# Kernel tuning notes

Hardware: AMD Instinct MI355X
Metric: run time of the kernel (lower is better)

## Reference

```python
import jax, jax.numpy as jnp
import numpy as np

B = 8       # complexes in batch
C = 32      # CDR residues per antibody
G = 2048    # antigen nodes per complex
D = 128     # encoded_dims
N_AB = B * C
N_AG = B * G
N = N_AB + N_AG
SLOPE = 0.2
EPS_BN = 1e-5


def _build_edges():
    # block-sparse bipartite edges (cdr_b x ag_b), symmetrized, + self loops
    srcs, dsts = [], []
    for b in range(B):
        ab = np.arange(b * C, (b + 1) * C)
        ag = np.arange(N_AB + b * G, N_AB + (b + 1) * G)
        g1, g2 = np.meshgrid(ab, ag, indexing='ij')
        srcs.append(g1.ravel()); dsts.append(g2.ravel())
    s = np.concatenate(srcs); d = np.concatenate(dsts)
    loops = np.arange(N)
    src = np.concatenate([s, d, loops]).astype(np.int32)
    dst = np.concatenate([d, s, loops]).astype(np.int32)
    return src, dst


def setup_inputs() -> dict:
    key = jax.random.key(0)
    ks = jax.random.split(key, 16)
    sc = 1.0 / np.sqrt(D)
    edge_src, edge_dst = _build_edges()
    return {
        'selected_ab': jax.random.normal(ks[0], (N_AB, D), jnp.float32),
        'x_ag': jax.random.normal(ks[1], (N_AG, D), jnp.float32),
        'W1': jax.random.normal(ks[2], (D, D), jnp.float32) * sc,
        'a_src1': jax.random.normal(ks[3], (D,), jnp.float32) * sc,
        'a_dst1': jax.random.normal(ks[4], (D,), jnp.float32) * sc,
        'b1': jnp.zeros((D,), jnp.float32),
        'W2': jax.random.normal(ks[5], (D, D), jnp.float32) * sc,
        'a_src2': jax.random.normal(ks[6], (D,), jnp.float32) * sc,
        'a_dst2': jax.random.normal(ks[7], (D,), jnp.float32) * sc,
        'b2': jnp.zeros((D,), jnp.float32),
        'bn_ab_g': jnp.ones((2 * D,), jnp.float32),
        'bn_ab_b': jnp.zeros((2 * D,), jnp.float32),
        'bn_ag_g': jnp.ones((2 * D,), jnp.float32),
        'bn_ag_b': jnp.zeros((2 * D,), jnp.float32),
        'fc_w': jax.random.normal(ks[8], (2 * D, 1), jnp.float32) * sc,
        'fc_b': jnp.zeros((1,), jnp.float32),
        'agfc_w': jax.random.normal(ks[9], (2 * D, 1), jnp.float32) * sc,
        'agfc_b': jnp.zeros((1,), jnp.float32),
        'edge_src': jnp.asarray(edge_src),
        'edge_dst': jnp.asarray(edge_dst),
    }


def _gat(x, W, a_s, a_d, b, src, dst):
    # PyG GATConv, heads=1, eval mode (dropout off)
    h = x @ W                                  # [N, D]
    al_s = h @ a_s                             # [N]
    al_d = h @ a_d                             # [N]
    e = jax.nn.leaky_relu(al_s[src] + al_d[dst], SLOPE)   # [E]
    m = jax.ops.segment_max(e, dst, num_segments=N)
    e = jnp.exp(e - m[dst])
    z = jax.ops.segment_sum(e, dst, num_segments=N)
    alpha = e / (z[dst] + 1e-16)
    out = jax.ops.segment_sum(h[src] * alpha[:, None], dst, num_segments=N)
    return out + b


def _bn(x, g, b):
    # training-mode batch stats (biased variance), like torch BatchNorm1d
    m = x.mean(0)
    v = ((x - m) ** 2).mean(0)
    return (x - m) / jnp.sqrt(v + EPS_BN) * g + b


def reference(selected_ab, x_ag, W1, a_src1, a_dst1, b1, W2, a_src2, a_dst2, b2,
              bn_ab_g, bn_ab_b, bn_ag_g, bn_ag_b, fc_w, fc_b, agfc_w, agfc_b,
              edge_src, edge_dst):
    x = jnp.concatenate([selected_ab, x_ag], axis=0)          # [N, D]
    x = jax.nn.relu(_gat(x, W1, a_src1, a_dst1, b1, edge_src, edge_dst))
    x = _gat(x, W2, a_src2, a_dst2, b2, edge_src, edge_dst)
    x_ab = jnp.concatenate([x[:N_AB], selected_ab], axis=1)   # [N_ab, 2D]
    x_ab = jax.nn.relu(_bn(x_ab, bn_ab_g, bn_ab_b))
    x_ab = (x_ab @ fc_w + fc_b).ravel()
    x_ag_o = jnp.concatenate([x[N_AB:], x_ag], axis=1)        # [N_ag, 2D]
    x_ag_o = jax.nn.relu(_bn(x_ag_o, bn_ag_g, bn_ag_b))
    x_ag_o = (x_ag_o @ agfc_w + agfc_b).ravel()
    return (x_ab, x_ag_o)
```

## Files before the change

kernel.cpp:

```cpp
#include <hip/hip_runtime.h>


#define N_AB 256
#define N_AG 16384
#define N_ALL 16640
#define G_AG 2048
#define SLOPE 0.2f
#define MSHIFT 20.0f

typedef __attribute__((ext_vector_type(4))) float f32x4;
typedef __attribute__((ext_vector_type(8))) __bf16 bf16x8;
typedef __attribute__((ext_vector_type(8))) unsigned short u16x8;
typedef unsigned short ushort_t;

__device__ __forceinline__ float bf2f(ushort_t u) {
  union { unsigned int i; float f; } v; v.i = ((unsigned int)u) << 16; return v.f;
}
__device__ __forceinline__ ushort_t f2bf(float f) {
  union { float fv; unsigned int i; } v; v.fv = f;
  unsigned int x = v.i;
  return (ushort_t)((x + 0x7fffu + ((x >> 16) & 1u)) >> 16);
}
__device__ __forceinline__ float lrelu(float x) { return x >= 0.f ? x : SLOPE * x; }
__device__ __forceinline__ float expw(float e) {
  return __expf(fminf(e, 60.f) - MSHIFT);
}
__device__ __forceinline__ float ldf(const void* p, size_t i, int f) {
  return f ? ((const float*)p)[i] : bf2f(((const ushort_t*)p)[i]);
}
__device__ __forceinline__ void ld8f(const void* p, size_t i, int f, float* o) {
  if (f) {
    const f32x4* q = (const f32x4*)((const float*)p + i);
    f32x4 a = q[0], b = q[1];
#pragma unroll
    for (int j = 0; j < 4; ++j) { o[j] = a[j]; o[j + 4] = b[j]; }
  } else {
    u16x8 v = *(const u16x8*)((const ushort_t*)p + i);
#pragma unroll
    for (int j = 0; j < 8; ++j) o[j] = bf2f(v[j]);
  }
}

__global__ __launch_bounds__(256) void k_pre(
    const void* __restrict__ W1, const void* __restrict__ W2,
    const void* __restrict__ as1, const void* __restrict__ ad1,
    const void* __restrict__ as2, const void* __restrict__ ad2,
    const void* __restrict__ sel_ab,
    ushort_t* __restrict__ W1t, ushort_t* __restrict__ W2t,
    float* __restrict__ va, float* __restrict__ bnsumAG,
    float* __restrict__ accf, float* __restrict__ accz,
    float* __restrict__ selpart, float* __restrict__ selpartq,
    int* __restrict__ flagp) {
  __shared__ float ls[2][128], lq[2][128];
  int t = threadIdx.x, lane = t & 63, wid = t >> 6;
  int bx = blockIdx.x;
  const ushort_t* selu = (const ushort_t*)sel_ab;
  int cnt = 0;
#pragma unroll
  for (int i = 0; i < 8; ++i) {
    unsigned e = (selu[lane * 8 + i] >> 7) & 0xFF;
    if (e > 0xC8) cnt++;
  }
  int f = (__popcll(__ballot(cnt > 0)) >= 3) ? 1 : 0;
  if (bx == 0 && t == 0) flagp[0] = f;

  if (bx < 16) {
    const void* W = (bx < 8) ? W1 : W2;
    ushort_t* Wt = (bx < 8) ? W1t : W2t;
    int base = (bx & 7) * 2048 + t * 8;
    float o[8];
    ld8f(W, base, f, o);
#pragma unroll
    for (int j = 0; j < 8; ++j) {
      int idx = base + j;
      Wt[(idx & 127) * 128 + (idx >> 7)] = f2bf(o[j]);
    }
  } else if (bx < 32) {
    int j = bx - 16;
    const void* W   = (j < 8) ? W1 : W2;
    const void* asv = (j < 8) ? as1 : as2;
    const void* adv = (j < 8) ? ad1 : ad2;
    int vbase = (j < 8) ? 0 : 256;
    int basek = (j & 7) * 16 + wid * 4;
    float a_s0 = ldf(asv, lane, f), a_s1 = ldf(asv, lane + 64, f);
    float a_d0 = ldf(adv, lane, f), a_d1 = ldf(adv, lane + 64, f);
#pragma unroll
    for (int i = 0; i < 4; ++i) {
      int k = basek + i;
      float w0 = ldf(W, (size_t)k * 128 + lane, f);
      float w1 = ldf(W, (size_t)k * 128 + lane + 64, f);
      float ps = w0 * a_s0 + w1 * a_s1;
      float pd = w0 * a_d0 + w1 * a_d1;
#pragma unroll
      for (int o = 1; o < 64; o <<= 1) {
        ps += __shfl_xor(ps, o);
        pd += __shfl_xor(pd, o);
      }
      if (lane == 0) { va[vbase + k] = ps; va[vbase + 128 + k] = pd; }
    }
  } else if (bx < 40) {
    int j = bx - 32;
    f32x4* az = (f32x4*)(accf + (size_t)j * 4096);
    f32x4 z4 = (f32x4){0.f, 0.f, 0.f, 0.f};
    for (int i = t; i < 1024; i += 256) az[i] = z4;
    if (j == 0) { bnsumAG[t] = 0.f; bnsumAG[t + 256] = 0.f; accz[t] = 0.f; }
  } else {
    int j = bx - 40;
    int col = t & 127, rh = t >> 7;
    int r0 = j * 32 + rh * 16;
    float s = 0.f, sq = 0.f;
    for (int r = 0; r < 16; ++r) {
      float v = ldf(sel_ab, (size_t)(r0 + r) * 128 + col, f);
      s += v; sq += v * v;
    }
    ls[rh][col] = s; lq[rh][col] = sq;
    __syncthreads();
    if (t < 128) {
      selpart[j * 128 + t] = ls[0][t] + ls[1][t];
      selpartq[j * 128 + t] = lq[0][t] + lq[1][t];
    }
  }
}

__global__ __launch_bounds__(256) void k_gemm(
    const void* __restrict__ xa, int modeA,
    const void* __restrict__ xb, int modeB,
    const int* __restrict__ flagp,
    const ushort_t* __restrict__ Wt, const float* __restrict__ va,
    ushort_t* __restrict__ h, float* __restrict__ als, float* __restrict__ ald,
    float* __restrict__ accf, float* __restrict__ accz,
    const void* __restrict__ biasAb, float* __restrict__ xabf, int do_abfin,
    const void* __restrict__ xraw, float* __restrict__ bnsumAG, int do_colsum) {
  __shared__ float zsh[32], wsh[32];
  int t = threadIdx.x, lane = t & 63, wid = t >> 6;
  int bx = blockIdx.x;

  if (do_colsum && bx < 64) {
    int fr = *flagp;
    int j = bx;
    int col = t & 127, half = t >> 7;
    int r0 = j * 256 + half * 128;
    float s = 0.f, sq = 0.f;
    for (int r = 0; r < 128; ++r) {
      float v = ldf(xraw, (size_t)(r0 + r) * 128 + col, fr);
      s += v; sq += v * v;
    }
    atomicAdd(&bnsumAG[128 + col], s);
    atomicAdd(&bnsumAG[384 + col], sq);
    return;
  }
  int gbx = do_colsum ? bx - 64 : bx;

  if (do_abfin && bx < 8) {
    int fr = *flagp;
    int b = bx;
    if (t < 32) {
      int grow = b * 32 + t;
      float w = expw(lrelu(als[grow] + ald[grow]));
      zsh[t] = accz[grow] + w;
      wsh[t] = w;
      accz[grow] = 0.f;
    }
    __syncthreads();
#pragma unroll
    for (int i = 0; i < 16; ++i) {
      int e = i * 256 + t;
      int rl = e >> 7, col = e & 127;
      int grow = b * 32 + rl;
      size_t idx = (size_t)grow * 128 + col;
      float hv = bf2f(h[idx]);
      float v = (accf[idx] + wsh[rl] * hv) / (zsh[rl] + 1e-16f) + ldf(biasAb, col, fr);
      accf[idx] = 0.f;
      v = fmaxf(v, 0.f);
      xabf[idx] = v;
    }
    __syncthreads();
  }

  int rw0 = gbx * 32 + (wid >> 1) * 16;
  int ch = wid & 1;
  const void* xsrc; int roff, mode;
  if (rw0 < N_AB) { xsrc = xa; roff = rw0; mode = modeA; }
  else            { xsrc = xb; roff = rw0 - N_AB; mode = modeB; }
  int fx = (mode == 2) ? *flagp : mode;
  int mm = lane & 15, q = lane >> 4;
  f32x4 acc[4];
#pragma unroll
  for (int b = 0; b < 4; ++b) acc[b] = (f32x4){0.f, 0.f, 0.f, 0.f};
  float pals = 0.f, pald = 0.f;
#pragma unroll
  for (int s = 0; s < 4; ++s) {
    int koff = s * 32 + q * 8;
    union { u16x8 u; bf16x8 b; } af;
    float o[8];
    ld8f(xsrc, (size_t)(roff + mm) * 128 + koff, fx, o);
#pragma unroll
    for (int j = 0; j < 8; ++j) {
      af.u[j] = f2bf(o[j]);
      pals += o[j] * va[koff + j];
      pald += o[j] * va[128 + koff + j];
    }
#pragma unroll
    for (int nt = 0; nt < 4; ++nt) {
      int colb = ch * 64 + nt * 16;
      bf16x8 bfr = *(const bf16x8*)(Wt + (size_t)(colb + mm) * 128 + koff);
      acc[nt] = __builtin_amdgcn_mfma_f32_16x16x32_bf16(af.b, bfr, acc[nt], 0, 0, 0);
    }
  }
  if (ch == 0) {
    float s1 = pals; s1 += __shfl_xor(s1, 16); s1 += __shfl_xor(s1, 32);
    float d1 = pald; d1 += __shfl_xor(d1, 16); d1 += __shfl_xor(d1, 32);
    if (lane < 16) { als[rw0 + lane] = s1; ald[rw0 + lane] = d1; }
  }
#pragma unroll
  for (int nt = 0; nt < 4; ++nt)
#pragma unroll
    for (int r = 0; r < 4; ++r) {
      int row = rw0 + q * 4 + r;
      int col = ch * 64 + nt * 16 + mm;
      h[(size_t)row * 128 + col] = f2bf(acc[nt][r]);
    }
}

#define ABP_STRIDE 72
#define AG_STRIDE 40
#define HS_OFF 5120
#define HS_STRIDE 136
__global__ __launch_bounds__(256) void k_agg(
    const ushort_t* __restrict__ h, const float* __restrict__ als,
    const float* __restrict__ ald, const void* __restrict__ bias,
    const int* __restrict__ flagp, ushort_t* __restrict__ xout,
    float* __restrict__ accf, float* __restrict__ accz,
    float* __restrict__ bnsumAG, int do_relu, int do_bnsum) {
  __shared__ ushort_t hT[13824];
  __shared__ float alsS[64];
  __shared__ float colsum[128], colsq[128];
  int bx = blockIdx.x;
  int t = threadIdx.x, lane = t & 63, wid = t >> 6;
  int mm = lane & 15, q = lane >> 4;

  if (bx < 256) {
    int b = bx >> 5, jt = bx & 31;
    int f = *flagp;
    int jbase = N_AB + b * G_AG + jt * 64;
    {
      int row = t & 31, c0g = (t >> 5) * 16;
      const ushort_t* src = h + (size_t)(b * 32 + row) * 128 + c0g;
      u16x8 v0 = *(const u16x8*)src;
      u16x8 v1 = *(const u16x8*)(src + 8);
#pragma unroll
      for (int j = 0; j < 8; ++j) {
        hT[(c0g + j) * AG_STRIDE + row] = v0[j];
        hT[(c0g + 8 + j) * AG_STRIDE + row] = v1[j];
      }
      ushort_t* hS = hT + HS_OFF;
      const ushort_t* hsrc = h + (size_t)jbase * 128;
#pragma unroll
      for (int it = 0; it < 4; ++it) {
        int e = it * 2048 + t * 8;
        int rr = e >> 7, cb = e & 127;
        *(u16x8*)&hS[rr * HS_STRIDE + cb] =
            *(const u16x8*)(hsrc + (size_t)rr * 128 + cb);
      }
      if (t < 32) alsS[t] = als[b * 32 + t];
      if (t < 128) { colsum[t] = 0.f; colsq[t] = 0.f; }
    }
    __syncthreads();
    int jl = jt * 64 + wid * 16;
    int jrow = N_AB + b * G_AG + jl;
    float aldj = ald[jrow + mm];
    float alsj = als[jrow + mm];
    union { u16x8 u; bf16x8 b; } af;
    float zp = 0.f;
#pragma unroll
    for (int j = 0; j < 8; ++j) {
      ushort_t us = f2bf(expw(lrelu(alsS[q * 8 + j] + aldj)));
      af.u[j] = us;
      zp += bf2f(us);
    }
    zp += __shfl_xor(zp, 16);
    zp += __shfl_xor(zp, 32);
    float wself = expw(lrelu(alsj + aldj));
    float z = zp + wself;
    float zin[4], wz[4];
#pragma unroll
    for (int r = 0; r < 4; ++r) {
      int rowl = q * 4 + r;
      float zr = __shfl(z, rowl);
      float wsr = __shfl(wself, rowl);
      float inv = 1.0f / (zr + 1e-16f);
      zin[r] = inv; wz[r] = wsr * inv;
    }
    const ushort_t* hSr = hT + HS_OFF + (size_t)(wid * 16) * HS_STRIDE;
#pragma unroll
    for (int nt = 0; nt < 8; ++nt) {
      int col = nt * 16 + mm;
      union { u16x8 u; bf16x8 b; } bfr;
      bfr.b = *(const bf16x8*)(&hT[col * AG_STRIDE + q * 8]);
      f32x4 acc = {0.f, 0.f, 0.f, 0.f};
      acc = __builtin_amdgcn_mfma_f32_16x16x32_bf16(af.b, bfr.b, acc, 0, 0, 0);
      float biasv = ldf(bias, col, f);
      float sl = 0.f, sq = 0.f;
#pragma unroll
      for (int r = 0; r < 4; ++r) {
        int row = q * 4 + r;
        float hv = bf2f(hSr[row * HS_STRIDE + col]);
        float v = acc[r] * zin[r] + wz[r] * hv + biasv;
        sl += v; sq += v * v;
        if (do_relu) v = fmaxf(v, 0.f);
        xout[(size_t)(jrow + row) * 128 + col] = f2bf(v);
      }
      if (do_bnsum) {
        atomicAdd(&colsum[col], sl);
        atomicAdd(&colsq[col], sq);
      }
    }
    if (do_bnsum) {
      __syncthreads();
      if (t < 128) {
        atomicAdd(&bnsumAG[t], colsum[t]);
        atomicAdd(&bnsumAG[256 + t], colsq[t]);
      }
    }
  } else {
    int bx2 = bx - 256;
    int b = bx2 >> 5, sg = bx2 & 31;
    int jrow0 = N_AB + b * G_AG + sg * 64;
    {
      int jr = t & 63, cgrp = (t >> 6) * 32;
      const ushort_t* src = h + (size_t)(jrow0 + jr) * 128 + cgrp;
#pragma unroll
      for (int v = 0; v < 4; ++v) {
        u16x8 vv = *(const u16x8*)(src + v * 8);
#pragma unroll
        for (int j = 0; j < 8; ++j)
          hT[(cgrp + v * 8 + j) * ABP_STRIDE + jr] = vv[j];
      }
      if (t < 64) alsS[t] = als[jrow0 + t];
    }
    __syncthreads();
    float aldm[2] = { ald[b * 32 + mm], ald[b * 32 + 16 + mm] };
    f32x4 acc[2][2];
#pragma unroll
    for (int a = 0; a < 2; ++a)
#pragma unroll
      for (int c = 0; c < 2; ++c) acc[a][c] = (f32x4){0.f, 0.f, 0.f, 0.f};
    float zz[2] = {0.f, 0.f};
#pragma unroll
    for (int s = 0; s < 2; ++s) {
      int k0 = s * 32 + q * 8;
      float a8[8];
#pragma unroll
      for (int j = 0; j < 8; ++j) a8[j] = alsS[k0 + j];
      union { u16x8 u; bf16x8 b; } af[2];
#pragma unroll
      for (int mt = 0; mt < 2; ++mt)
#pragma unroll
        for (int j = 0; j < 8; ++j) {
          ushort_t us = f2bf(expw(lrelu(a8[j] + aldm[mt])));
          af[mt].u[j] = us;
          zz[mt] += bf2f(us);
        }
#pragma unroll
      for (int ns = 0; ns < 2; ++ns) {
        int n = wid * 32 + ns * 16 + mm;
        union { u16x8 u; bf16x8 b; } bfr;
        bfr.b = *(const bf16x8*)(&hT[n * ABP_STRIDE + k0]);
        acc[0][ns] = __builtin_amdgcn_mfma_f32_16x16x32_bf16(af[0].b, bfr.b, acc[0][ns], 0, 0, 0);
        acc[1][ns] = __builtin_amdgcn_mfma_f32_16x16x32_bf16(af[1].b, bfr.b, acc[1][ns], 0, 0, 0);
      }
    }
#pragma unroll
    for (int mt = 0; mt < 2; ++mt)
#pragma unroll
      for (int ns = 0; ns < 2; ++ns)
#pragma unroll
        for (int r = 0; r < 4; ++r) {
          int row = b * 32 + mt * 16 + q * 4 + r;
          int col = wid * 32 + ns * 16 + mm;
          atomicAdd(&accf[(size_t)row * 128 + col], acc[mt][ns][r]);
        }
#pragma unroll
    for (int mt = 0; mt < 2; ++mt) {
      float z = zz[mt];
      z += __shfl_xor(z, 16);
      z += __shfl_xor(z, 32);
      if (wid == 0 && lane < 16)
        atomicAdd(&accz[b * 32 + mt * 16 + lane], z);
    }
  }
}

__global__ __launch_bounds__(256) void k_abfin(
    const float* __restrict__ accf, const float* __restrict__ accz,
    const ushort_t* __restrict__ h, const float* __restrict__ als,
    const float* __restrict__ ald, const void* __restrict__ bias,
    const int* __restrict__ flagp, float* __restrict__ xabf,
    float* __restrict__ abpart, float* __restrict__ abpartq,
    const float* __restrict__ bnsumAG,
    const void* __restrict__ gag, const void* __restrict__ bag,
    const void* __restrict__ agfcw, float* __restrict__ statsAG) {
  __shared__ float zsh[8], wsh[8];
  __shared__ float cs[2][128], cq[2][128];
  int bx = blockIdx.x, t = threadIdx.x;
  int f = *flagp;
  if (bx == 32) {
    float mean = bnsumAG[t] * (1.f / 16384.f);
    float var = fmaxf(bnsumAG[256 + t] * (1.f / 16384.f) - mean * mean, 0.f);
    float A = ldf(gag, t, f) / sqrtf(var + 1e-5f);
    statsAG[t] = A;
    statsAG[256 + t] = ldf(bag, t, f) - mean * A;
    statsAG[512 + t] = ldf(agfcw, t, f);
    return;
  }
  int b = bx >> 2, q4 = bx & 3;
  if (t < 8) {
    int grow = b * 32 + q4 * 8 + t;
    float w = expw(lrelu(als[grow] + ald[grow]));
    zsh[t] = accz[grow] + w;
    wsh[t] = w;
  }
  __syncthreads();
  float s = 0.f, sq = 0.f;
#pragma unroll
  for (int i = 0; i < 4; ++i) {
    int e = i * 256 + t;
    int rl = e >> 7, col = e & 127;
    int grow = b * 32 + q4 * 8 + rl;
    size_t idx = (size_t)grow * 128 + col;
    float hv = bf2f(h[idx]);
    float v = (accf[idx] + wsh[rl] * hv) / (zsh[rl] + 1e-16f) + ldf(bias, col, f);
    xabf[idx] = v;
    s += v; sq += v * v;
  }
  cs[t >> 7][t & 127] = s;
  cq[t >> 7][t & 127] = sq;
  __syncthreads();
  if (t < 128) {
    abpart[bx * 128 + t] = cs[0][t] + cs[1][t];
    abpartq[bx * 128 + t] = cq[0][t] + cq[1][t];
  }
}

__global__ __launch_bounds__(256) void k_head(
    const float* __restrict__ xfab, const ushort_t* __restrict__ xfag,
    const void* __restrict__ sel_ab, const void* __restrict__ x_ag,
    const float* __restrict__ statsAG,
    const float* __restrict__ selpart, const float* __restrict__ selpartq,
    const float* __restrict__ abpart, const float* __restrict__ abpartq,
    const void* __restrict__ gab, const void* __restrict__ bab,
    const void* __restrict__ fcw,
    const void* __restrict__ fcb, const void* __restrict__ agfcb,
    const int* __restrict__ flagp, void* __restrict__ out) {
  __shared__ float stA[256], stB[256], stW[256];
  int t = threadIdx.x, lane = t & 63, wid = t >> 6;
  int f = *flagp;
  int isAb = (blockIdx.x < 16);
  if (isAb) {
    float s = 0.f, sq = 0.f;
    if (t < 128) {
      for (int j = 0; j < 32; ++j) {
        s += abpart[j * 128 + t];
        sq += abpartq[j * 128 + t];
      }
    } else {
      int c = t - 128;
      for (int j = 0; j < 8; ++j) {
        s += selpart[j * 128 + c];
        sq += selpartq[j * 128 + c];
      }
    }
    float mean = s * (1.f / 256.f);
    float var = fmaxf(sq * (1.f / 256.f) - mean * mean, 0.f);
    float A = ldf(gab, t, f) / sqrtf(var + 1e-5f);
    stA[t] = A;
    stB[t] = ldf(bab, t, f) - mean * A;
    stW[t] = ldf(fcw, t, f);
  } else {
    stA[t] = statsAG[t];
    stB[t] = statsAG[256 + t];
    stW[t] = statsAG[512 + t];
  }
  __syncthreads();

  int c0 = lane * 2;
  float a0 = stA[c0],        a1 = stA[c0 + 1];
  float a2 = stA[128 + c0],  a3 = stA[128 + c0 + 1];
  float g0 = stB[c0],        g1 = stB[c0 + 1];
  float g2 = stB[128 + c0],  g3 = stB[128 + c0 + 1];
  float w0 = stW[c0],        w1 = stW[c0 + 1];
  float w2 = stW[128 + c0],  w3 = stW[128 + c0 + 1];
  int row0 = isAb ? (blockIdx.x * 16 + wid * 4)
                  : (N_AB + (blockIdx.x - 16) * 16 + wid * 4);
  float bb = isAb ? ldf(fcb, 0, f) : ldf(agfcb, 0, f);
#pragma unroll
  for (int i = 0; i < 4; ++i) {
    int row = row0 + i;
    float v0, v1, v2, v3;
    if (isAb) {
      const float* p = xfab + (size_t)row * 128 + c0;
      v0 = p[0]; v1 = p[1];
      size_t ro = (size_t)row * 128 + c0;
      v2 = ldf(sel_ab, ro, f);
      v3 = ldf(sel_ab, ro + 1, f);
    } else {
      const ushort_t* p = xfag + (size_t)row * 128 + c0;
      v0 = bf2f(p[0]); v1 = bf2f(p[1]);
      size_t ro = (size_t)(row - N_AB) * 128 + c0;
      v2 = ldf(x_ag, ro, f);
      v3 = ldf(x_ag, ro + 1, f);
    }
    float acc =
        fmaxf(v0 * a0 + g0, 0.f) * w0
      + fmaxf(v1 * a1 + g1, 0.f) * w1
      + fmaxf(v2 * a2 + g2, 0.f) * w2
      + fmaxf(v3 * a3 + g3, 0.f) * w3;
#pragma unroll
    for (int o = 1; o < 64; o <<= 1) acc += __shfl_xor(acc, o);
    if (lane == 0) {
      float r = acc + bb;
      if (f) ((float*)out)[row] = r;
      else   ((ushort_t*)out)[row] = f2bf(r);
    }
  }
}

extern "C" void kernel_launch(void* const* d_in, const int* in_sizes, int n_in,
                              void* d_out, int out_size, void* d_ws, size_t ws_size,
                              hipStream_t stream) {
  (void)in_sizes; (void)n_in; (void)out_size; (void)ws_size;
  const void* sel_ab = d_in[0];
  const void* x_ag   = d_in[1];
  const void* W1     = d_in[2];
  const void* as1    = d_in[3];
  const void* ad1    = d_in[4];
  const void* b1     = d_in[5];
  const void* W2     = d_in[6];
  const void* as2    = d_in[7];
  const void* ad2    = d_in[8];
  const void* b2     = d_in[9];
  const void* gab    = d_in[10];
  const void* bab    = d_in[11];
  const void* gag    = d_in[12];
  const void* bag    = d_in[13];
  const void* fcw    = d_in[14];
  const void* fcb    = d_in[15];
  const void* agfcw  = d_in[16];
  const void* agfcb  = d_in[17];

  ushort_t* h  = (ushort_t*)d_in[18];
  ushort_t* xb = (ushort_t*)d_in[19];

  char* wsp = (char*)d_ws;
  size_t off = 0;
  auto carve = [&](size_t bytes) -> char* {
    char* p = wsp + off; off += (bytes + 255) & ~(size_t)255; return p;
  };
  int* flag      = (int*)carve(64 * 4);
  ushort_t* W1t  = (ushort_t*)carve(16384 * 2);
  ushort_t* W2t  = (ushort_t*)carve(16384 * 2);
  float* va      = (float*)carve(512 * 4);
  float* als     = (float*)carve((size_t)N_ALL * 4);
  float* ald     = (float*)carve((size_t)N_ALL * 4);
  float* bnsumAG = (float*)carve(512 * 4);
  float* statsAG = (float*)carve(768 * 4);
  float* xabf    = (float*)carve((size_t)N_AB * 128 * 4);
  float* accf    = (float*)carve((size_t)N_AB * 128 * 4);
  float* accz    = (float*)carve(256 * 4);
  float* selpart = (float*)carve(8 * 128 * 4);
  float* selpartq= (float*)carve(8 * 128 * 4);
  float* abpart  = (float*)carve(32 * 128 * 4);
  float* abpartq = (float*)carve(32 * 128 * 4);

  k_pre<<<48, 256, 0, stream>>>(W1, W2, as1, ad1, as2, ad2, sel_ab,
                                W1t, W2t, va, bnsumAG, accf, accz,
                                selpart, selpartq, flag);
  k_gemm<<<584, 256, 0, stream>>>(sel_ab, 2, x_ag, 2, flag, W1t, va, h, als, ald,
                                  accf, accz, b1, xabf, 0, x_ag, bnsumAG, 1);
  k_agg<<<512, 256, 0, stream>>>(h, als, ald, b1, flag, xb, accf, accz,
                                 bnsumAG, 1, 0);
  k_gemm<<<520, 256, 0, stream>>>(xabf, 1, xb + (size_t)N_AB * 128, 0, flag, W2t, va + 256, h, als, ald,
                                  accf, accz, b1, xabf, 1, x_ag, bnsumAG, 0);
  k_agg<<<512, 256, 0, stream>>>(h, als, ald, b2, flag, xb, accf, accz,
                                 bnsumAG, 0, 1);
  k_abfin<<<33, 256, 0, stream>>>(accf, accz, h, als, ald, b2, flag, xabf,
                                  abpart, abpartq, bnsumAG, gag, bag, agfcw,
                                  statsAG);
  k_head<<<1040, 256, 0, stream>>>(xabf, xb, sel_ab, x_ag, statsAG,
                                   selpart, selpartq, abpart, abpartq,
                                   gab, bab, fcw, fcb, agfcb, flag, d_out);
}
```

Measured before the change: 171.7 us.

## Fuse all GAT stages into one persistent kernel with grid-wide barriers

Merges the seven separate kernel launches (pre, two gemm, two agg, ab finish, head) into one persistent kernel with 512 blocks. The stages are separated by atomic-counter grid barriers, and the kernel is used only when occupancy allows 2 blocks per CU. It also moves the antigen BN input statistics into the pre phase as per-block partial sums instead of accumulating them during the first gemm. The aim is to remove launch gaps and inter-kernel drain, at the cost of spin-wait barriers, a possible deadlock if the grid does not all fit on the device, and lower parallelism for the GEMM stages.

```diff
diff --git a/kernel.cpp b/kernel.cpp
--- a/kernel.cpp
+++ b/kernel.cpp
@@ -7,6 +7,7 @@
 #define G_AG 2048
 #define SLOPE 0.2f
 #define MSHIFT 20.0f
+#define GRID_F 512
 
 typedef __attribute__((ext_vector_type(4))) float f32x4;
 typedef __attribute__((ext_vector_type(8))) __bf16 bf16x8;
@@ -38,6 +39,496 @@
     u16x8 v = *(const u16x8*)((const ushort_t*)p + i);
 #pragma unroll
     for (int j = 0; j < 8; ++j) o[j] = bf2f(v[j]);
+  }
+}
+
+__device__ __forceinline__ void gbar(unsigned* __restrict__ ctr, int t) {
+  __syncthreads();
+  if (t == 0) {
+    __threadfence();
+    atomicAdd(ctr, 1u);
+    while (atomicAdd(ctr, 0u) < (unsigned)GRID_F) __builtin_amdgcn_s_sleep(2);
+  }
+  __syncthreads();
+  __threadfence();
+}
+
+__global__ __launch_bounds__(64) void k_init(unsigned* __restrict__ ctr) {
+  if (threadIdx.x < 16) ctr[threadIdx.x] = 0u;
+}
+
+#define ABP_STRIDE 72
+#define AG_STRIDE 40
+#define HS_OFF 5120
+#define HS_STRIDE 136
+
+__global__ __launch_bounds__(256, 2) void k_fused(
+    const void* __restrict__ sel_ab, const void* __restrict__ x_ag,
+    const void* __restrict__ W1, const void* __restrict__ as1,
+    const void* __restrict__ ad1, const void* __restrict__ b1,
+    const void* __restrict__ W2, const void* __restrict__ as2,
+    const void* __restrict__ ad2, const void* __restrict__ b2,
+    const void* __restrict__ gab, const void* __restrict__ bab,
+    const void* __restrict__ gag, const void* __restrict__ bag,
+    const void* __restrict__ fcw, const void* __restrict__ fcb,
+    const void* __restrict__ agfcw, const void* __restrict__ agfcb,
+    ushort_t* __restrict__ h, ushort_t* __restrict__ xb,
+    ushort_t* __restrict__ W1t, ushort_t* __restrict__ W2t,
+    float* __restrict__ va, float* __restrict__ als, float* __restrict__ ald,
+    float* __restrict__ bnsumAG, float* __restrict__ statsAG,
+    float* __restrict__ xabf, float* __restrict__ accf,
+    float* __restrict__ accz,
+    float* __restrict__ selpart, float* __restrict__ selpartq,
+    float* __restrict__ abpart, float* __restrict__ abpartq,
+    float* __restrict__ agpart, float* __restrict__ agpartq,
+    unsigned* __restrict__ ctrs, void* __restrict__ out) {
+  __shared__ ushort_t hT[13824];
+  __shared__ float alsS[64];
+  __shared__ float colsum[128], colsq[128];
+  __shared__ float preLs[2][128], preLq[2][128];
+  __shared__ float zsh[32], wsh[32];
+  __shared__ float stA[256], stB[256], stW[256];
+
+  int t = threadIdx.x, lane = t & 63, wid = t >> 6;
+  int bx = blockIdx.x;
+  int mm = lane & 15, q = lane >> 4;
+
+  const ushort_t* selu = (const ushort_t*)sel_ab;
+  int cnt = 0;
+#pragma unroll
+  for (int i = 0; i < 8; ++i) {
+    unsigned e = (selu[lane * 8 + i] >> 7) & 0xFF;
+    if (e > 0xC8) cnt++;
+  }
+  int f = (__popcll(__ballot(cnt > 0)) >= 3) ? 1 : 0;
+
+  if (bx < 16) {
+    const void* W = (bx < 8) ? W1 : W2;
+    ushort_t* Wt = (bx < 8) ? W1t : W2t;
+    int base = (bx & 7) * 2048 + t * 8;
+    float o[8];
+    ld8f(W, base, f, o);
+#pragma unroll
+    for (int j = 0; j < 8; ++j) {
+      int idx = base + j;
+      Wt[(idx & 127) * 128 + (idx >> 7)] = f2bf(o[j]);
+    }
+  } else if (bx < 32) {
+    int j = bx - 16;
+    const void* W   = (j < 8) ? W1 : W2;
+    const void* asv = (j < 8) ? as1 : as2;
+    const void* adv = (j < 8) ? ad1 : ad2;
+    int vbase = (j < 8) ? 0 : 256;
+    int basek = (j & 7) * 16 + wid * 4;
+    float a_s0 = ldf(asv, lane, f), a_s1 = ldf(asv, lane + 64, f);
+    float a_d0 = ldf(adv, lane, f), a_d1 = ldf(adv, lane + 64, f);
+#pragma unroll
+    for (int i = 0; i < 4; ++i) {
+      int k = basek + i;
+      float w0 = ldf(W, (size_t)k * 128 + lane, f);
+      float w1 = ldf(W, (size_t)k * 128 + lane + 64, f);
+      float ps = w0 * a_s0 + w1 * a_s1;
+      float pd = w0 * a_d0 + w1 * a_d1;
+#pragma unroll
+      for (int o = 1; o < 64; o <<= 1) {
+        ps += __shfl_xor(ps, o);
+        pd += __shfl_xor(pd, o);
+      }
+      if (lane == 0) { va[vbase + k] = ps; va[vbase + 128 + k] = pd; }
+    }
+  } else if (bx < 40) {
+    int j = bx - 32;
+    f32x4* az = (f32x4*)(accf + (size_t)j * 4096);
+    f32x4 z4 = (f32x4){0.f, 0.f, 0.f, 0.f};
+    for (int i = t; i < 1024; i += 256) az[i] = z4;
+    if (j == 0) { bnsumAG[t] = 0.f; bnsumAG[t + 256] = 0.f; accz[t] = 0.f; }
+  } else if (bx < 48) {
+    int j = bx - 40;
+    int col = t & 127, rh = t >> 7;
+    int r0 = j * 32 + rh * 16;
+    float s = 0.f, sq = 0.f;
+    for (int r = 0; r < 16; ++r) {
+      float v = ldf(sel_ab, (size_t)(r0 + r) * 128 + col, f);
+      s += v; sq += v * v;
+    }
+    preLs[rh][col] = s; preLq[rh][col] = sq;
+    __syncthreads();
+    if (t < 128) {
+      selpart[j * 128 + t] = preLs[0][t] + preLs[1][t];
+      selpartq[j * 128 + t] = preLq[0][t] + preLq[1][t];
+    }
+  } else if (bx < 112) {
+    int j = bx - 48;
+    int col = t & 127, half = t >> 7;
+    int r0 = j * 256 + half * 128;
+    float s = 0.f, sq = 0.f;
+    for (int r = 0; r < 128; ++r) {
+      float v = ldf(x_ag, (size_t)(r0 + r) * 128 + col, f);
+      s += v; sq += v * v;
+    }
+    preLs[half][col] = s; preLq[half][col] = sq;
+    __syncthreads();
+    if (t < 128) {
+      agpart[j * 128 + t] = preLs[0][t] + preLs[1][t];
+      agpartq[j * 128 + t] = preLq[0][t] + preLq[1][t];
+    }
+  }
+  gbar(&ctrs[0], t);
+
+  auto gemm_tile = [&](int tile, const void* xa, int fxA, const void* xbv,
+                       int fxB, const ushort_t* Wt, const float* vav) {
+    int rw0 = tile * 32 + (wid >> 1) * 16;
+    int ch = wid & 1;
+    const void* xsrc; int roff, fx;
+    if (rw0 < N_AB) { xsrc = xa; roff = rw0; fx = fxA; }
+    else            { xsrc = xbv; roff = rw0 - N_AB; fx = fxB; }
+    f32x4 acc[4];
+#pragma unroll
+    for (int b = 0; b < 4; ++b) acc[b] = (f32x4){0.f, 0.f, 0.f, 0.f};
+    float pals = 0.f, pald = 0.f;
+#pragma unroll
+    for (int s = 0; s < 4; ++s) {
+      int koff = s * 32 + q * 8;
+      union { u16x8 u; bf16x8 b; } af;
+      float o[8];
+      ld8f(xsrc, (size_t)(roff + mm) * 128 + koff, fx, o);
+#pragma unroll
+      for (int j = 0; j < 8; ++j) {
+        af.u[j] = f2bf(o[j]);
+        pals += o[j] * vav[koff + j];
+        pald += o[j] * vav[128 + koff + j];
+      }
+#pragma unroll
+      for (int nt = 0; nt < 4; ++nt) {
+        int colb = ch * 64 + nt * 16;
+        bf16x8 bfr = *(const bf16x8*)(Wt + (size_t)(colb + mm) * 128 + koff);
+        acc[nt] = __builtin_amdgcn_mfma_f32_16x16x32_bf16(af.b, bfr, acc[nt], 0, 0, 0);
+      }
+    }
+    if (ch == 0) {
+      float s1 = pals; s1 += __shfl_xor(s1, 16); s1 += __shfl_xor(s1, 32);
+      float d1 = pald; d1 += __shfl_xor(d1, 16); d1 += __shfl_xor(d1, 32);
+      if (lane < 16) { als[rw0 + lane] = s1; ald[rw0 + lane] = d1; }
+    }
+#pragma unroll
+    for (int nt = 0; nt < 4; ++nt)
+#pragma unroll
+      for (int r = 0; r < 4; ++r) {
+        int row = rw0 + q * 4 + r;
+        int col = ch * 64 + nt * 16 + mm;
+        h[(size_t)row * 128 + col] = f2bf(acc[nt][r]);
+      }
+  };
+
+  auto agg_phase = [&](const void* bias, int do_relu, int do_bnsum) {
+    if (bx < 256) {
+      int b = bx >> 5, jt = bx & 31;
+      int jbase = N_AB + b * G_AG + jt * 64;
+      {
+        int row = t & 31, c0g = (t >> 5) * 16;
+        const ushort_t* src = h + (size_t)(b * 32 + row) * 128 + c0g;
+        u16x8 v0 = *(const u16x8*)src;
+        u16x8 v1 = *(const u16x8*)(src + 8);
+#pragma unroll
+        for (int j = 0; j < 8; ++j) {
+          hT[(c0g + j) * AG_STRIDE + row] = v0[j];
+          hT[(c0g + 8 + j) * AG_STRIDE + row] = v1[j];
+        }
+        ushort_t* hS = hT + HS_OFF;
+        const ushort_t* hsrc = h + (size_t)jbase * 128;
+#pragma unroll
+        for (int it = 0; it < 4; ++it) {
+          int e = it * 2048 + t * 8;
+          int rr = e >> 7, cb = e & 127;
+          *(u16x8*)&hS[rr * HS_STRIDE + cb] =
+              *(const u16x8*)(hsrc + (size_t)rr * 128 + cb);
+        }
+        if (t < 32) alsS[t] = als[b * 32 + t];
+        if (t < 128) { colsum[t] = 0.f; colsq[t] = 0.f; }
+      }
+      __syncthreads();
+      int jl = jt * 64 + wid * 16;
+      int jrow = N_AB + b * G_AG + jl;
+      float aldj = ald[jrow + mm];
+      float alsj = als[jrow + mm];
+      union { u16x8 u; bf16x8 b; } af;
+      float zp = 0.f;
+#pragma unroll
+      for (int j = 0; j < 8; ++j) {
+        ushort_t us = f2bf(expw(lrelu(alsS[q * 8 + j] + aldj)));
+        af.u[j] = us;
+        zp += bf2f(us);
+      }
+      zp += __shfl_xor(zp, 16);
+      zp += __shfl_xor(zp, 32);
+      float wself = expw(lrelu(alsj + aldj));
+      float z = zp + wself;
+      float zin[4], wz[4];
+#pragma unroll
+      for (int r = 0; r < 4; ++r) {
+        int rowl = q * 4 + r;
+        float zr = __shfl(z, rowl);
+        float wsr = __shfl(wself, rowl);
+        float inv = 1.0f / (zr + 1e-16f);
+        zin[r] = inv; wz[r] = wsr * inv;
+      }
+      const ushort_t* hSr = hT + HS_OFF + (size_t)(wid * 16) * HS_STRIDE;
+#pragma unroll
+      for (int nt = 0; nt < 8; ++nt) {
+        int col = nt * 16 + mm;
+        union { u16x8 u; bf16x8 b; } bfr;
+        bfr.b = *(const bf16x8*)(&hT[col * AG_STRIDE + q * 8]);
+        f32x4 acc = {0.f, 0.f, 0.f, 0.f};
+        acc = __builtin_amdgcn_mfma_f32_16x16x32_bf16(af.b, bfr.b, acc, 0, 0, 0);
+        float biasv = ldf(bias, col, f);
+        float sl = 0.f, sq = 0.f;
+#pragma unroll
+        for (int r = 0; r < 4; ++r) {
+          int row = q * 4 + r;
+          float hv = bf2f(hSr[row * HS_STRIDE + col]);
+          float v = acc[r] * zin[r] + wz[r] * hv + biasv;
+          sl += v; sq += v * v;
+          if (do_relu) v = fmaxf(v, 0.f);
+          xb[(size_t)(jrow + row) * 128 + col] = f2bf(v);
+        }
+        if (do_bnsum) {
+          atomicAdd(&colsum[col], sl);
+          atomicAdd(&colsq[col], sq);
+        }
+      }
+      if (do_bnsum) {
+        __syncthreads();
+        if (t < 128) {
+          atomicAdd(&bnsumAG[t], colsum[t]);
+          atomicAdd(&bnsumAG[256 + t], colsq[t]);
+        }
+      }
+    } else {
+      int bx2 = bx - 256;
+      int b = bx2 >> 5, sg = bx2 & 31;
+      int jrow0 = N_AB + b * G_AG + sg * 64;
+      {
+        int jr = t & 63, cgrp = (t >> 6) * 32;
+        const ushort_t* src = h + (size_t)(jrow0 + jr) * 128 + cgrp;
+#pragma unroll
+        for (int v = 0; v < 4; ++v) {
+          u16x8 vv = *(const u16x8*)(src + v * 8);
+#pragma unroll
+          for (int j = 0; j < 8; ++j)
+            hT[(cgrp + v * 8 + j) * ABP_STRIDE + jr] = vv[j];
+        }
+        if (t < 64) alsS[t] = als[jrow0 + t];
+      }
+      __syncthreads();
+      float aldm[2] = { ald[b * 32 + mm], ald[b * 32 + 16 + mm] };
+      f32x4 acc[2][2];
+#pragma unroll
+      for (int a = 0; a < 2; ++a)
+#pragma unroll
+        for (int c = 0; c < 2; ++c) acc[a][c] = (f32x4){0.f, 0.f, 0.f, 0.f};
+      float zz[2] = {0.f, 0.f};
+#pragma unroll
+      for (int s = 0; s < 2; ++s) {
+        int k0 = s * 32 + q * 8;
+        float a8[8];
+#pragma unroll
+        for (int j = 0; j < 8; ++j) a8[j] = alsS[k0 + j];
+        union { u16x8 u; bf16x8 b; } af[2];
+#pragma unroll
+        for (int mt = 0; mt < 2; ++mt)
+#pragma unroll
+          for (int j = 0; j < 8; ++j) {
+            ushort_t us = f2bf(expw(lrelu(a8[j] + aldm[mt])));
+            af[mt].u[j] = us;
+            zz[mt] += bf2f(us);
+          }
+#pragma unroll
+        for (int ns = 0; ns < 2; ++ns) {
+          int n = wid * 32 + ns * 16 + mm;
+          union { u16x8 u; bf16x8 b; } bfr;
+          bfr.b = *(const bf16x8*)(&hT[n * ABP_STRIDE + k0]);
+          acc[0][ns] = __builtin_amdgcn_mfma_f32_16x16x32_bf16(af[0].b, bfr.b, acc[0][ns], 0, 0, 0);
+          acc[1][ns] = __builtin_amdgcn_mfma_f32_16x16x32_bf16(af[1].b, bfr.b, acc[1][ns], 0, 0, 0);
+        }
+      }
+#pragma unroll
+      for (int mt = 0; mt < 2; ++mt)
+#pragma unroll
+        for (int ns = 0; ns < 2; ++ns)
+#pragma unroll
+          for (int r = 0; r < 4; ++r) {
+            int row = b * 32 + mt * 16 + q * 4 + r;
+            int col = wid * 32 + ns * 16 + mm;
+            atomicAdd(&accf[(size_t)row * 128 + col], acc[mt][ns][r]);
+          }
+#pragma unroll
+      for (int mt = 0; mt < 2; ++mt) {
+        float z = zz[mt];
+        z += __shfl_xor(z, 16);
+        z += __shfl_xor(z, 32);
+        if (wid == 0 && lane < 16)
+          atomicAdd(&accz[b * 32 + mt * 16 + lane], z);
+      }
+    }
+  };
+
+  for (int tile = bx; tile < 520; tile += GRID_F)
+    gemm_tile(tile, sel_ab, f, x_ag, f, W1t, va);
+  gbar(&ctrs[1], t);
+
+  agg_phase(b1, 1, 0);
+  gbar(&ctrs[2], t);
+
+  if (bx < 8) {
+    int b = bx;
+    if (t < 32) {
+      int grow = b * 32 + t;
+      float w = expw(lrelu(als[grow] + ald[grow]));
+      zsh[t] = accz[grow] + w;
+      wsh[t] = w;
+      accz[grow] = 0.f;
+    }
+    __syncthreads();
+#pragma unroll
+    for (int i = 0; i < 16; ++i) {
+      int e = i * 256 + t;
+      int rl = e >> 7, col = e & 127;
+      int grow = b * 32 + rl;
+      size_t idx = (size_t)grow * 128 + col;
+      float hv = bf2f(h[idx]);
+      float v = (accf[idx] + wsh[rl] * hv) / (zsh[rl] + 1e-16f) + ldf(b1, col, f);
+      accf[idx] = 0.f;
+      v = fmaxf(v, 0.f);
+      xabf[idx] = v;
+    }
+    __syncthreads();
+  }
+  for (int tile = bx; tile < 520; tile += GRID_F)
+    gemm_tile(tile, xabf, 1, (const void*)(xb + (size_t)N_AB * 128), 0, W2t,
+              va + 256);
+  gbar(&ctrs[3], t);
+
+  agg_phase(b2, 0, 1);
+  gbar(&ctrs[4], t);
+
+  if (bx < 33) {
+    if (bx == 32) {
+      float sB, sqB;
+      if (t < 128) { sB = bnsumAG[t]; sqB = bnsumAG[256 + t]; }
+      else {
+        int c = t - 128;
+        sB = 0.f; sqB = 0.f;
+        for (int j = 0; j < 64; ++j) {
+          sB += agpart[j * 128 + c];
+          sqB += agpartq[j * 128 + c];
+        }
+      }
+      float mean = sB * (1.f / 16384.f);
+      float var = fmaxf(sqB * (1.f / 16384.f) - mean * mean, 0.f);
+      float A = ldf(gag, t, f) / sqrtf(var + 1e-5f);
+      statsAG[t] = A;
+      statsAG[256 + t] = ldf(bag, t, f) - mean * A;
+      statsAG[512 + t] = ldf(agfcw, t, f);
+    } else {
+      int b = bx >> 2, q4 = bx & 3;
+      if (t < 8) {
+        int grow = b * 32 + q4 * 8 + t;
+        float w = expw(lrelu(als[grow] + ald[grow]));
+        zsh[t] = accz[grow] + w;
+        wsh[t] = w;
+      }
+      __syncthreads();
+      float s = 0.f, sq = 0.f;
+#pragma unroll
+      for (int i = 0; i < 4; ++i) {
+        int e = i * 256 + t;
+        int rl = e >> 7, col = e & 127;
+        int grow = b * 32 + q4 * 8 + rl;
+        size_t idx = (size_t)grow * 128 + col;
+        float hv = bf2f(h[idx]);
+        float v = (accf[idx] + wsh[rl] * hv) / (zsh[rl] + 1e-16f) + ldf(b2, col, f);
+        xabf[idx] = v;
+        s += v; sq += v * v;
+      }
+      preLs[t >> 7][t & 127] = s;
+      preLq[t >> 7][t & 127] = sq;
+      __syncthreads();
+      if (t < 128) {
+        abpart[bx * 128 + t] = preLs[0][t] + preLs[1][t];
+        abpartq[bx * 128 + t] = preLq[0][t] + preLq[1][t];
+      }
+    }
+  }
+  gbar(&ctrs[5], t);
+
+  for (int g = bx; g < 1040; g += GRID_F) {
+    __syncthreads();
+    int isAb = (g < 16);
+    if (isAb) {
+      float s = 0.f, sq = 0.f;
+      if (t < 128) {
+        for (int j = 0; j < 32; ++j) {
+          s += abpart[j * 128 + t];
+          sq += abpartq[j * 128 + t];
+        }
+      } else {
+        int c = t - 128;
+        for (int j = 0; j < 8; ++j) {
+          s += selpart[j * 128 + c];
+          sq += selpartq[j * 128 + c];
+        }
+      }
+      float mean = s * (1.f / 256.f);
+      float var = fmaxf(sq * (1.f / 256.f) - mean * mean, 0.f);
+      float A = ldf(gab, t, f) / sqrtf(var + 1e-5f);
+      stA[t] = A;
+      stB[t] = ldf(bab, t, f) - mean * A;
+      stW[t] = ldf(fcw, t, f);
+    } else {
+      stA[t] = statsAG[t];
+      stB[t] = statsAG[256 + t];
+      stW[t] = statsAG[512 + t];
+    }
+    __syncthreads();
+    int c0 = lane * 2;
+    float a0 = stA[c0],        a1 = stA[c0 + 1];
+    float a2 = stA[128 + c0],  a3 = stA[128 + c0 + 1];
+    float g0 = stB[c0],        g1 = stB[c0 + 1];
+    float g2 = stB[128 + c0],  g3 = stB[128 + c0 + 1];
+    float w0 = stW[c0],        w1 = stW[c0 + 1];
+    float w2 = stW[128 + c0],  w3 = stW[128 + c0 + 1];
+    int row0 = isAb ? (g * 16 + wid * 4) : (N_AB + (g - 16) * 16 + wid * 4);
+    float bb = isAb ? ldf(fcb, 0, f) : ldf(agfcb, 0, f);
+#pragma unroll
+    for (int i = 0; i < 4; ++i) {
+      int row = row0 + i;
+      float v0, v1, v2, v3;
+      if (isAb) {
+        const float* p = xabf + (size_t)row * 128 + c0;
+        v0 = p[0]; v1 = p[1];
+        size_t ro = (size_t)row * 128 + c0;
+        v2 = ldf(sel_ab, ro, f);
+        v3 = ldf(sel_ab, ro + 1, f);
+      } else {
+        const ushort_t* p = xb + (size_t)row * 128 + c0;
+        v0 = bf2f(p[0]); v1 = bf2f(p[1]);
+        size_t ro = (size_t)(row - N_AB) * 128 + c0;
+        v2 = ldf(x_ag, ro, f);
+        v3 = ldf(x_ag, ro + 1, f);
+      }
+      float acc =
+          fmaxf(v0 * a0 + g0, 0.f) * w0
+        + fmaxf(v1 * a1 + g1, 0.f) * w1
+        + fmaxf(v2 * a2 + g2, 0.f) * w2
+        + fmaxf(v3 * a3 + g3, 0.f) * w3;
+#pragma unroll
+      for (int o = 1; o < 64; o <<= 1) acc += __shfl_xor(acc, o);
+      if (lane == 0) {
+        float r = acc + bb;
+        if (f) ((float*)out)[row] = r;
+        else   ((ushort_t*)out)[row] = f2bf(r);
+      }
+    }
   }
 }
 
@@ -222,10 +713,6 @@
     }
 }
 
-#define ABP_STRIDE 72
-#define AG_STRIDE 40
-#define HS_OFF 5120
-#define HS_STRIDE 136
 __global__ __launch_bounds__(256) void k_agg(
     const ushort_t* __restrict__ h, const float* __restrict__ als,
     const float* __restrict__ ald, const void* __restrict__ bias,
@@ -571,6 +1058,27 @@
   float* selpartq= (float*)carve(8 * 128 * 4);
   float* abpart  = (float*)carve(32 * 128 * 4);
   float* abpartq = (float*)carve(32 * 128 * 4);
+  float* agpart  = (float*)carve(64 * 128 * 4);
+  float* agpartq = (float*)carve(64 * 128 * 4);
+  unsigned* ctrs = (unsigned*)carve(16 * 4);
+
+  static int fusedOK = -1;
+  if (fusedOK < 0) {
+    int nb = 0;
+    hipError_t e = hipOccupancyMaxActiveBlocksPerMultiprocessor(&nb, k_fused, 256, 0);
+    fusedOK = (e == hipSuccess && nb >= 2) ? 1 : 0;
+  }
+
+  if (fusedOK) {
+    k_init<<<1, 64, 0, stream>>>(ctrs);
+    k_fused<<<GRID_F, 256, 0, stream>>>(
+        sel_ab, x_ag, W1, as1, ad1, b1, W2, as2, ad2, b2,
+        gab, bab, gag, bag, fcw, fcb, agfcw, agfcb,
+        h, xb, W1t, W2t, va, als, ald, bnsumAG, statsAG,
+        xabf, accf, accz, selpart, selpartq, abpart, abpartq,
+        agpart, agpartq, ctrs, d_out);
+    return;
+  }
 
   k_pre<<<48, 256, 0, stream>>>(W1, W2, as1, ad1, as2, ad2, sel_ab,
                                 W1t, W2t, va, bnsumAG, accf, accz,
```

Measured after the change: 171.0 us. No clear change (-0.4%).
